# Kernel optimization log

Measured on AMD Instinct MI355X. Metric: run time of the kernel, lower is better.

The kernel has to match this reference:

```python
import jax, jax.numpy as jnp
import numpy as np

LATENT = 10
MAXLEN = 80
DT = 0.1
STEPS = int(round(1.0 / DT))
HIDDEN = 32
BATCH = 512


def _score_fn(xt_bld, time_b1, W1, b1, W2, b2):
    # score_model: flatten (B, L, D) -> concat time -> Dense(32, relu) -> Dense(D)
    B = xt_bld.shape[0]
    h = jnp.concatenate([xt_bld.reshape(B, -1), time_b1], axis=-1)  # (B, L*D+1)
    h = jax.nn.relu(h @ W1 + b1)
    return h @ W2 + b2  # (B, D)


def setup_inputs() -> dict:
    key = jax.random.key(0)
    k1, k2, k3, k4 = jax.random.split(key, 4)
    fan_in = MAXLEN * LATENT + 1  # 801
    z_mean = jax.random.normal(k1, (BATCH, MAXLEN, LATENT), jnp.float32)
    z_log_var = 0.1 * jax.random.normal(k2, (BATCH, MAXLEN, LATENT), jnp.float32)
    W1 = jax.random.normal(k3, (fan_in, HIDDEN), jnp.float32) / np.sqrt(fan_in)
    b1 = jnp.zeros((HIDDEN,), jnp.float32)
    W2 = jax.random.normal(k4, (HIDDEN, LATENT), jnp.float32) / np.sqrt(HIDDEN)
    b2 = jnp.zeros((LATENT,), jnp.float32)
    return {"z_mean": z_mean, "z_log_var": z_log_var, "W1": W1, "b1": b1, "W2": W2, "b2": b2}


def _diffusion_loss(z_mean, z_log_var, W1, b1, W2, b2):
    B = z_mean.shape[0]
    sigma = jnp.exp(z_log_var)                    # ez_log_var in train_step
    mu_tr = jnp.transpose(z_mean, (1, 0, 2))      # (L, B, D)
    sigma_tr = jnp.transpose(sigma, (1, 0, 2))    # (L, B, D)
    zero = jnp.zeros((1, B, LATENT), mu_tr.dtype)
    full_mu_ext = jnp.concatenate([zero, mu_tr], axis=0)       # (L+1, B, D)
    full_sigma_ext = jnp.concatenate([zero, sigma_tr], axis=0)  # (L+1, B, D)
    noise_keys = jax.random.split(jax.random.key(1337), MAXLEN * (STEPS + 1)).reshape(MAXLEN, STEPS + 1)

    def diffusion_step(i, mu_i, sigma_i, keys):
        # mask_below_target_step: keep rows < i
        mask = (jnp.arange(MAXLEN) < i).astype(mu_tr.dtype)[:, None, None]
        masked_mu = mu_tr * mask                                   # (L, B, D)
        times = i.astype(jnp.float32) + jnp.arange(STEPS, dtype=jnp.float32) * DT
        sigma_std = jnp.sqrt(sigma_i)                              # (B, D)
        x0 = mu_i + sigma_std * jax.random.normal(keys[0], (B, LATENT))

        def body(xt, xs):
            t, k = xs
            t_idx = jnp.floor(t).astype(jnp.int32)
            next_mu = jax.lax.dynamic_index_in_dim(full_mu_ext, t_idx + 1, 0, keepdims=False)
            next_sigma = jax.lax.dynamic_index_in_dim(full_sigma_ext, t_idx + 1, 0, keepdims=False)
            one_hot = jax.nn.one_hot(t_idx, MAXLEN, dtype=xt.dtype)     # (L,)
            score_in = masked_mu + one_hot[:, None, None] * xt[None]    # (L, B, D)
            score_in = jnp.transpose(score_in, (1, 0, 2))               # (B, L, D)
            time_col = jnp.full((B, 1), t, xt.dtype)
            score = _score_fn(score_in, time_col, W1, b1, W2, b2)       # (B, D)
            logdx = -(xt - next_mu) / jnp.sqrt(next_sigma)
            err = jnp.abs(logdx - score)
            dW = jax.random.normal(k, (B, LATENT)) * jnp.sqrt(DT)
            xt = xt + 0.5 * jnp.square(sigma_std) * score + sigma_std * dW
            return xt, err

        xt_final, errs = jax.lax.scan(body, x0, (times, keys[1:]))
        return xt_final, errs.sum(axis=0)  # tf.reduce_sum(error, axis=0)

    seq, err = jax.vmap(diffusion_step)(jnp.arange(MAXLEN), mu_tr, sigma_tr, noise_keys)
    sequence = jnp.transpose(seq, (1, 0, 2))       # (B, L, D)
    score_error = jnp.transpose(err, (1, 0, 2))    # (B, L, D)
    return sequence, score_error


def reference(z_mean, z_log_var, W1, b1, W2, b2):
    return _diffusion_loss(z_mean, z_log_var, W1, b1, W2, b2)
```

## Files before the change

### kernel.cpp

```cpp
#include <hip/hip_runtime.h>
#include <stdint.h>

#define LATENT 10
#define MAXLEN 80
#define STEPS  10
#define HIDDEN 32
#define BATCH  512
#define NSEG   16
#define SEGL   5
#define CPB    16
#define TPB    128

__device__ __forceinline__ void tf2x32(uint32_t k0, uint32_t k1,
                                       uint32_t x0, uint32_t x1,
                                       uint32_t& o0, uint32_t& o1) {
  uint32_t ks2 = k0 ^ k1 ^ 0x1BD11BDAu;
  uint32_t v0 = x0 + k0;
  uint32_t v1 = x1 + k1;
#define TF_R(rot) { v0 += v1; v1 = (v1 << (rot)) | (v1 >> (32 - (rot))); v1 ^= v0; }
  TF_R(13) TF_R(15) TF_R(26) TF_R(6)
  v0 += k1;  v1 += ks2 + 1u;
  TF_R(17) TF_R(29) TF_R(16) TF_R(24)
  v0 += ks2; v1 += k0 + 2u;
  TF_R(13) TF_R(15) TF_R(26) TF_R(6)
  v0 += k0;  v1 += k1 + 3u;
  TF_R(17) TF_R(29) TF_R(16) TF_R(24)
  v0 += k1;  v1 += ks2 + 4u;
  TF_R(13) TF_R(15) TF_R(26) TF_R(6)
  v0 += ks2; v1 += k0 + 5u;
#undef TF_R
  o0 = v0; o1 = v1;
}

__device__ __forceinline__ float bits_to_normal(uint32_t bits) {
  const float lo = -0.99999994f;
  float f = __uint_as_float((bits >> 9) | 0x3f800000u) - 1.0f;
  float u = fmaf(f, 2.0f, lo);
  u = fmaxf(u, lo);
  float w = -__logf(fmaf(-u, u, 1.0f));
  float p;
  if (w < 5.0f) {
    w -= 2.5f;
    p = 2.81022636e-08f;
    p = fmaf(p, w, 3.43273939e-07f);
    p = fmaf(p, w, -3.5233877e-06f);
    p = fmaf(p, w, -4.39150654e-06f);
    p = fmaf(p, w, 0.00021858087f);
    p = fmaf(p, w, -0.00125372503f);
    p = fmaf(p, w, -0.00417768164f);
    p = fmaf(p, w, 0.246640727f);
    p = fmaf(p, w, 1.50140941f);
  } else {
    w = sqrtf(w) - 3.0f;
    p = -0.000200214257f;
    p = fmaf(p, w, 0.000100950558f);
    p = fmaf(p, w, 0.00134934322f);
    p = fmaf(p, w, -0.00367342844f);
    p = fmaf(p, w, 0.00573950773f);
    p = fmaf(p, w, -0.0076224613f);
    p = fmaf(p, w, 0.00943887047f);
    p = fmaf(p, w, 1.00167406f);
    p = fmaf(p, w, 2.83297682f);
  }
  return 1.4142135623730951f * (p * u);
}

__global__ __launch_bounds__(256) void k_seg(
    const float* __restrict__ zmean, const float* __restrict__ W1,
    float* __restrict__ segtot) {
  int id = blockIdx.x * 256 + threadIdx.x;
  int s = id >> 14;
  int r = id & 16383;
  int b = r >> 5, j = r & 31;
  float pf0 = 0.0f, pf1 = 0.0f;
#pragma unroll
  for (int t = 0; t < SEGL; ++t) {
    int l = s * SEGL + t;
    const float2* mrow = (const float2*)(zmean + (b * MAXLEN + l) * LATENT);
    float2 m0 = mrow[0], m1 = mrow[1], m2 = mrow[2], m3 = mrow[3], m4 = mrow[4];
    const float* wl = W1 + (l * LATENT) * HIDDEN + j;
    pf0 = fmaf(m0.x, wl[0 * HIDDEN], pf0);
    pf1 = fmaf(m0.y, wl[1 * HIDDEN], pf1);
    pf0 = fmaf(m1.x, wl[2 * HIDDEN], pf0);
    pf1 = fmaf(m1.y, wl[3 * HIDDEN], pf1);
    pf0 = fmaf(m2.x, wl[4 * HIDDEN], pf0);
    pf1 = fmaf(m2.y, wl[5 * HIDDEN], pf1);
    pf0 = fmaf(m3.x, wl[6 * HIDDEN], pf0);
    pf1 = fmaf(m3.y, wl[7 * HIDDEN], pf1);
    pf0 = fmaf(m4.x, wl[8 * HIDDEN], pf0);
    pf1 = fmaf(m4.y, wl[9 * HIDDEN], pf1);
  }
  segtot[(s * BATCH + b) * HIDDEN + j] = pf0 + pf1;
}

__global__ __launch_bounds__(TPB) void k_chain(
    const float* __restrict__ zmean, const float* __restrict__ zlv,
    const float* __restrict__ W1, const float* __restrict__ b1v,
    const float* __restrict__ W2, const float* __restrict__ b2v,
    const float* __restrict__ segtot,
    float* __restrict__ outSeq, float* __restrict__ outErr) {
  __shared__ float nrmS[(STEPS + 1) * LATENT * CPB];
  __shared__ uint32_t skk[2 * (STEPS + 1)];

  const int tid = threadIdx.x;
  const int i = blockIdx.x >> 5;
  const int b0 = (blockIdx.x & 31) << 4;

  if (tid < (STEPS + 1)) {
    uint32_t a, c;
    tf2x32(0u, 1337u, 0u, (uint32_t)(i * (STEPS + 1) + tid), a, c);
    skk[2 * tid] = a; skk[2 * tid + 1] = c;
  }
  __syncthreads();

  const float SQRT_DT = 0.31622776601683794f;
#define GEN_DRAW(IDX)                                                        \
  {                                                                          \
    int c_ = (IDX) & (CPB - 1), n_ = (IDX) >> 4;                             \
    int k_ = (n_ * 205) >> 11;                                               \
    int d_ = n_ - k_ * 10;                                                   \
    uint32_t o0_, o1_;                                                       \
    tf2x32(skk[2 * k_], skk[2 * k_ + 1], 0u,                                 \
           (uint32_t)((b0 + c_) * LATENT + d_), o0_, o1_);                   \
    float v_ = bits_to_normal(o0_ ^ o1_);                                    \
    nrmS[n_ * CPB + c_] = (n_ < LATENT) ? v_ : v_ * SQRT_DT;                 \
  }
#pragma unroll
  for (int rr = 0; rr < 13; ++rr) GEN_DRAW(rr * TPB + tid);
  if (tid < (STEPS + 1) * LATENT * CPB - 13 * TPB) GEN_DRAW(13 * TPB + tid);
#undef GEN_DRAW
  __syncthreads();

  const int r = tid & 7;
  const int jb = r * 4;
  const int cloc = tid >> 3;
  const int b = b0 + cloc;

  const float* rowT = W1 + (MAXLEN * LATENT) * HIDDEN;
  float pf[4], wT[4];
  const float fi = (float)i;
#pragma unroll
  for (int k = 0; k < 4; ++k) {
    wT[k] = rowT[jb + k];
    pf[k] = fmaf(fi, wT[k], b1v[jb + k]);
  }
  const int fs = i / SEGL;
  for (int s2 = 0; s2 < fs; ++s2) {
    float4 t0 = *(const float4*)(segtot + ((size_t)s2 * BATCH + b) * HIDDEN + jb);
    pf[0] += t0.x; pf[1] += t0.y; pf[2] += t0.z; pf[3] += t0.w;
  }
  for (int l = fs * SEGL; l < i; ++l) {
    const float2* mrow = (const float2*)(zmean + (b * MAXLEN + l) * LATENT);
    const float* wl = W1 + (l * LATENT) * HIDDEN + jb;
#pragma unroll
    for (int p = 0; p < 5; ++p) {
      float2 m = mrow[p];
      float4 wa = *(const float4*)(wl + (2 * p) * HIDDEN);
      float4 wb = *(const float4*)(wl + (2 * p + 1) * HIDDEN);
      pf[0] = fmaf(m.x, wa.x, pf[0]); pf[1] = fmaf(m.x, wa.y, pf[1]);
      pf[2] = fmaf(m.x, wa.z, pf[2]); pf[3] = fmaf(m.x, wa.w, pf[3]);
      pf[0] = fmaf(m.y, wb.x, pf[0]); pf[1] = fmaf(m.y, wb.y, pf[1]);
      pf[2] = fmaf(m.y, wb.z, pf[2]); pf[3] = fmaf(m.y, wb.w, pf[3]);
    }
  }

  const int base = (b * MAXLEN + i) * LATENT;
  float mu[LATENT], shalf[LATENT], u[LATENT], errs[LATENT], b2[LATENT];
  float w1s[LATENT][4];
  {
    const float2* zm = (const float2*)(zmean + base);
    const float2* zl = (const float2*)(zlv + base);
    const float* W1i = W1 + (i * LATENT) * HIDDEN + jb;
#pragma unroll
    for (int p = 0; p < 5; ++p) {
      float2 m = zm[p], v = zl[p];
      float s0 = sqrtf(expf(v.x));
      float s1 = sqrtf(expf(v.y));
      mu[2 * p] = m.x; mu[2 * p + 1] = m.y;
      shalf[2 * p] = 0.5f * s0; shalf[2 * p + 1] = 0.5f * s1;
      float4 wa = *(const float4*)(W1i + (2 * p) * HIDDEN);
      float4 wb = *(const float4*)(W1i + (2 * p + 1) * HIDDEN);
      pf[0] = fmaf(m.x, wa.x, pf[0]); pf[1] = fmaf(m.x, wa.y, pf[1]);
      pf[2] = fmaf(m.x, wa.z, pf[2]); pf[3] = fmaf(m.x, wa.w, pf[3]);
      pf[0] = fmaf(m.y, wb.x, pf[0]); pf[1] = fmaf(m.y, wb.y, pf[1]);
      pf[2] = fmaf(m.y, wb.z, pf[2]); pf[3] = fmaf(m.y, wb.w, pf[3]);
      w1s[2 * p][0] = s0 * wa.x; w1s[2 * p][1] = s0 * wa.y;
      w1s[2 * p][2] = s0 * wa.z; w1s[2 * p][3] = s0 * wa.w;
      w1s[2 * p + 1][0] = s1 * wb.x; w1s[2 * p + 1][1] = s1 * wb.y;
      w1s[2 * p + 1][2] = s1 * wb.z; w1s[2 * p + 1][3] = s1 * wb.w;
    }
  }
#pragma unroll
  for (int d = 0; d < LATENT; ++d) {
    b2[d] = b2v[d];
    errs[d] = 0.0f;
    u[d] = nrmS[d * CPB + cloc];
  }

  const float* W2q = W2 + jb * LATENT;

  for (int s = 0; s < STEPS; ++s) {
    float nd[LATENT];
#pragma unroll
    for (int d = 0; d < LATENT; ++d)
      nd[d] = nrmS[((s + 1) * LATENT + d) * CPB + cloc];

    const float ts = (float)s * 0.1f;
    float h[4];
#pragma unroll
    for (int k = 0; k < 4; ++k) h[k] = fmaf(ts, wT[k], pf[k]);
#pragma unroll
    for (int d = 0; d < LATENT; ++d) {
      const float ud = u[d];
      h[0] = fmaf(ud, w1s[d][0], h[0]); h[1] = fmaf(ud, w1s[d][1], h[1]);
      h[2] = fmaf(ud, w1s[d][2], h[2]); h[3] = fmaf(ud, w1s[d][3], h[3]);
    }
    float sc[LATENT];
#pragma unroll
    for (int d = 0; d < LATENT; ++d) sc[d] = 0.0f;
#pragma unroll
    for (int k = 0; k < 4; ++k) {
      const float hj = fmaxf(h[k], 0.0f);
      const float2* w2r = (const float2*)(W2q + k * LATENT);
#pragma unroll
      for (int p = 0; p < 5; ++p) {
        float2 w = w2r[p];
        sc[2 * p] = fmaf(hj, w.x, sc[2 * p]);
        sc[2 * p + 1] = fmaf(hj, w.y, sc[2 * p + 1]);
      }
    }
#pragma unroll
    for (int m = 1; m < 8; m <<= 1) {
#pragma unroll
      for (int d = 0; d < LATENT; ++d) sc[d] += __shfl_xor(sc[d], m);
    }
#pragma unroll
    for (int d = 0; d < LATENT; ++d) {
      float st = sc[d] + b2[d];
      errs[d] += fabsf(u[d] + st);
      u[d] = u[d] + fmaf(shalf[d], st, nd[d]);
    }
  }

#pragma unroll
  for (int d = 0; d < LATENT; ++d) {
    if ((d & 7) == r) {
      float sd = shalf[d] + shalf[d];
      outSeq[base + d] = fmaf(sd, u[d], mu[d]);
      outErr[base + d] = errs[d];
    }
  }
}

__global__ __launch_bounds__(64) void k_mono(
    const float* __restrict__ zmean, const float* __restrict__ zlv,
    const float* __restrict__ W1, const float* __restrict__ b1v,
    const float* __restrict__ W2, const float* __restrict__ b2v,
    float* __restrict__ outSeq, float* __restrict__ outErr) {
  int i = blockIdx.x >> 3;
  int b = ((blockIdx.x & 7) << 6) + threadIdx.x;
  float pref[HIDDEN];
#pragma unroll
  for (int j = 0; j < HIDDEN; ++j) pref[j] = 0.0f;
  for (int l = 0; l < i; ++l) {
    const float* mrow = zmean + (b * MAXLEN + l) * LATENT;
    const float* wrow = W1 + (l * LATENT) * HIDDEN;
#pragma unroll
    for (int d = 0; d < LATENT; ++d) {
      float m = mrow[d];
#pragma unroll
      for (int j = 0; j < HIDDEN; ++j) pref[j] = fmaf(m, wrow[d * HIDDEN + j], pref[j]);
    }
  }
  const int base = (b * MAXLEN + i) * LATENT;
  float mu[LATENT], sstd[LATENT], xt[LATENT], errs[LATENT];
#pragma unroll
  for (int d = 0; d < LATENT; ++d) {
    mu[d] = zmean[base + d];
    sstd[d] = sqrtf(expf(zlv[base + d]));
  }
  float n0[LATENT];
  {
    uint32_t a, c;
    tf2x32(0u, 1337u, 0u, (uint32_t)(i * (STEPS + 1)), a, c);
#pragma unroll
    for (int d = 0; d < LATENT; ++d) {
      uint32_t o0, o1;
      tf2x32(a, c, 0u, (uint32_t)(b * LATENT + d), o0, o1);
      n0[d] = bits_to_normal(o0 ^ o1);
    }
  }
#pragma unroll
  for (int d = 0; d < LATENT; ++d) { xt[d] = mu[d] + sstd[d] * n0[d]; errs[d] = 0.0f; }
  const float* rowT  = W1 + (MAXLEN * LATENT) * HIDDEN;
  const float* rowsI = W1 + (i * LATENT) * HIDDEN;
  const float SQRT_DT = 0.31622776601683794f;
  for (int s = 0; s < STEPS; ++s) {
    float t = (float)i + (float)s * 0.1f;
    float h[HIDDEN];
#pragma unroll
    for (int j = 0; j < HIDDEN; ++j) h[j] = pref[j];
#pragma unroll
    for (int d = 0; d < LATENT; ++d) {
      float xd = xt[d];
      const float* row = rowsI + d * HIDDEN;
#pragma unroll
      for (int j = 0; j < HIDDEN; ++j) h[j] = fmaf(xd, row[j], h[j]);
    }
    float sc[LATENT];
#pragma unroll
    for (int d = 0; d < LATENT; ++d) sc[d] = b2v[d];
#pragma unroll
    for (int j = 0; j < HIDDEN; ++j) {
      float hj = fmaf(t, rowT[j], h[j]) + b1v[j];
      hj = fmaxf(hj, 0.0f);
      const float* w2r = W2 + j * LATENT;
#pragma unroll
      for (int d = 0; d < LATENT; ++d) sc[d] = fmaf(hj, w2r[d], sc[d]);
    }
    float nd[LATENT];
    {
      uint32_t a, c;
      tf2x32(0u, 1337u, 0u, (uint32_t)(i * (STEPS + 1) + s + 1), a, c);
#pragma unroll
      for (int d = 0; d < LATENT; ++d) {
        uint32_t o0, o1;
        tf2x32(a, c, 0u, (uint32_t)(b * LATENT + d), o0, o1);
        nd[d] = bits_to_normal(o0 ^ o1);
      }
    }
#pragma unroll
    for (int d = 0; d < LATENT; ++d) {
      float logdx = -(xt[d] - mu[d]) / sstd[d];
      errs[d] += fabsf(logdx - sc[d]);
      float dW = nd[d] * SQRT_DT;
      xt[d] = xt[d] + (0.5f * (sstd[d] * sstd[d])) * sc[d] + sstd[d] * dW;
    }
  }
#pragma unroll
  for (int d = 0; d < LATENT; ++d) {
    outSeq[base + d] = xt[d];
    outErr[base + d] = errs[d];
  }
}

extern "C" void kernel_launch(void* const* d_in, const int* in_sizes, int n_in,
                              void* d_out, int out_size, void* d_ws, size_t ws_size,
                              hipStream_t stream) {
  (void)in_sizes; (void)n_in; (void)out_size;
  const float* zmean = (const float*)d_in[0];
  const float* zlv   = (const float*)d_in[1];
  const float* W1    = (const float*)d_in[2];
  const float* b1v   = (const float*)d_in[3];
  const float* W2    = (const float*)d_in[4];
  const float* b2v   = (const float*)d_in[5];
  float* outSeq = (float*)d_out;
  float* outErr = outSeq + (size_t)BATCH * MAXLEN * LATENT;

  const size_t segBytes = (size_t)NSEG * BATCH * HIDDEN * sizeof(float);

  if (ws_size >= segBytes) {
    float* segtot = (float*)d_ws;
    hipLaunchKernelGGL(k_seg, dim3(NSEG * BATCH * HIDDEN / 256), dim3(256), 0, stream,
                       zmean, W1, segtot);
    hipLaunchKernelGGL(k_chain, dim3(MAXLEN * (BATCH / CPB)), dim3(TPB), 0, stream,
                       zmean, zlv, W1, b1v, W2, b2v, segtot, outSeq, outErr);
  } else {
    hipLaunchKernelGGL(k_mono, dim3(MAXLEN * 8), dim3(64), 0, stream,
                       zmean, zlv, W1, b1v, W2, b2v, outSeq, outErr);
  }
}
```

Baseline: 104.8 us.

## Replace shuffle butterfly reduction with LDS transpose-reduce and distribute latent ownership

Each group of 8 lanes used to all-reduce 10 score partials with a 3-level xor-shuffle butterfly (30 shuffles per step) and every lane redundantly updated all 10 latent dims. Now each lane writes its partials to shared memory and reads back 8 partials for only the one or two dims it owns, sums them, updates u, and publishes u to shared memory for the next step's hidden-layer accumulation. The per-column sigma is also precomputed once into shared memory rather than recomputed per thread. This trades shuffle traffic and redundant math for LDS round-trips. It relies on the 8 lanes sharing a column being in the same wavefront, since there is no barrier between the LDS writes and reads.

Measured after the change: 100.8 us. 3.8% less time.

```diff
diff --git a/kernel.cpp b/kernel.cpp
--- a/kernel.cpp
+++ b/kernel.cpp
@@ -10,6 +10,9 @@
 #define SEGL   5
 #define CPB    16
 #define TPB    128
+
+#define SCP_STRIDE 84
+#define US_STRIDE  12
 
 __device__ __forceinline__ void tf2x32(uint32_t k0, uint32_t k1,
                                        uint32_t x0, uint32_t x1,
@@ -101,6 +104,9 @@
     float* __restrict__ outSeq, float* __restrict__ outErr) {
   __shared__ float nrmS[(STEPS + 1) * LATENT * CPB];
   __shared__ uint32_t skk[2 * (STEPS + 1)];
+  __shared__ float shS[CPB * LATENT];
+  __shared__ float scP[CPB * SCP_STRIDE];
+  __shared__ float uS[CPB * US_STRIDE];
 
   const int tid = threadIdx.x;
   const int i = blockIdx.x >> 5;
@@ -110,6 +116,10 @@
     uint32_t a, c;
     tf2x32(0u, 1337u, 0u, (uint32_t)(i * (STEPS + 1) + tid), a, c);
     skk[2 * tid] = a; skk[2 * tid + 1] = c;
+  }
+  for (int t = tid; t < CPB * LATENT; t += TPB) {
+    int c_ = t / LATENT, d_ = t - c_ * LATENT;
+    shS[t] = 0.5f * sqrtf(expf(zlv[((b0 + c_) * MAXLEN + i) * LATENT + d_]));
   }
   __syncthreads();
 
@@ -165,19 +175,17 @@
   }
 
   const int base = (b * MAXLEN + i) * LATENT;
-  float mu[LATENT], shalf[LATENT], u[LATENT], errs[LATENT], b2[LATENT];
   float w1s[LATENT][4];
   {
     const float2* zm = (const float2*)(zmean + base);
-    const float2* zl = (const float2*)(zlv + base);
+    const float2* shp = (const float2*)(shS + cloc * LATENT);
     const float* W1i = W1 + (i * LATENT) * HIDDEN + jb;
 #pragma unroll
     for (int p = 0; p < 5; ++p) {
-      float2 m = zm[p], v = zl[p];
-      float s0 = sqrtf(expf(v.x));
-      float s1 = sqrtf(expf(v.y));
-      mu[2 * p] = m.x; mu[2 * p + 1] = m.y;
-      shalf[2 * p] = 0.5f * s0; shalf[2 * p + 1] = 0.5f * s1;
+      float2 m = zm[p];
+      float2 sh = shp[p];
+      float s0 = sh.x + sh.x;
+      float s1 = sh.y + sh.y;
       float4 wa = *(const float4*)(W1i + (2 * p) * HIDDEN);
       float4 wb = *(const float4*)(W1i + (2 * p + 1) * HIDDEN);
       pf[0] = fmaf(m.x, wa.x, pf[0]); pf[1] = fmaf(m.x, wa.y, pf[1]);
@@ -190,37 +198,56 @@
       w1s[2 * p + 1][2] = s1 * wb.z; w1s[2 * p + 1][3] = s1 * wb.w;
     }
   }
-#pragma unroll
-  for (int d = 0; d < LATENT; ++d) {
-    b2[d] = b2v[d];
-    errs[d] = 0.0f;
-    u[d] = nrmS[d * CPB + cloc];
+
+  float sh0 = shS[cloc * LATENT + r];
+  float b2o0 = b2v[r];
+  float u0o = nrmS[r * CPB + cloc];
+  float e0 = 0.0f;
+  float sh1 = 0.0f, b2o1 = 0.0f, u1o = 0.0f, e1 = 0.0f;
+  if (r < 2) {
+    sh1 = shS[cloc * LATENT + 8 + r];
+    b2o1 = b2v[8 + r];
+    u1o = nrmS[(8 + r) * CPB + cloc];
+  }
+  {
+    float* uw = uS + cloc * US_STRIDE;
+    uw[r] = u0o;
+    if (r < 2) uw[8 + r] = u1o;
   }
 
   const float* W2q = W2 + jb * LATENT;
+  float* scw = scP + cloc * SCP_STRIDE + r;
+  const float* scrd0 = scP + cloc * SCP_STRIDE + r * 8;
+  const float* scrd1 = scP + cloc * SCP_STRIDE + (8 + r) * 8;
+  const float2* urd = (const float2*)(uS + cloc * US_STRIDE);
+  const float* ndp = nrmS + LATENT * CPB + cloc;
 
   for (int s = 0; s < STEPS; ++s) {
-    float nd[LATENT];
-#pragma unroll
-    for (int d = 0; d < LATENT; ++d)
-      nd[d] = nrmS[((s + 1) * LATENT + d) * CPB + cloc];
+    float2 ua = urd[0], ub = urd[1], uc = urd[2], ud = urd[3], ue = urd[4];
 
     const float ts = (float)s * 0.1f;
     float h[4];
 #pragma unroll
     for (int k = 0; k < 4; ++k) h[k] = fmaf(ts, wT[k], pf[k]);
-#pragma unroll
-    for (int d = 0; d < LATENT; ++d) {
-      const float ud = u[d];
-      h[0] = fmaf(ud, w1s[d][0], h[0]); h[1] = fmaf(ud, w1s[d][1], h[1]);
-      h[2] = fmaf(ud, w1s[d][2], h[2]); h[3] = fmaf(ud, w1s[d][3], h[3]);
-    }
+#define ACC(d, val) { h[0] = fmaf((val), w1s[d][0], h[0]); h[1] = fmaf((val), w1s[d][1], h[1]); \
+                      h[2] = fmaf((val), w1s[d][2], h[2]); h[3] = fmaf((val), w1s[d][3], h[3]); }
+    ACC(0, ua.x) ACC(1, ua.y) ACC(2, ub.x) ACC(3, ub.y) ACC(4, uc.x)
+    ACC(5, uc.y) ACC(6, ud.x) ACC(7, ud.y) ACC(8, ue.x) ACC(9, ue.y)
+#undef ACC
+
     float sc[LATENT];
-#pragma unroll
-    for (int d = 0; d < LATENT; ++d) sc[d] = 0.0f;
-#pragma unroll
-    for (int k = 0; k < 4; ++k) {
-      const float hj = fmaxf(h[k], 0.0f);
+    {
+      float hj = fmaxf(h[0], 0.0f);
+      const float2* w2r = (const float2*)(W2q);
+#pragma unroll
+      for (int p = 0; p < 5; ++p) {
+        float2 w = w2r[p];
+        sc[2 * p] = hj * w.x; sc[2 * p + 1] = hj * w.y;
+      }
+    }
+#pragma unroll
+    for (int k = 1; k < 4; ++k) {
+      float hj = fmaxf(h[k], 0.0f);
       const float2* w2r = (const float2*)(W2q + k * LATENT);
 #pragma unroll
       for (int p = 0; p < 5; ++p) {
@@ -229,25 +256,46 @@
         sc[2 * p + 1] = fmaf(hj, w.y, sc[2 * p + 1]);
       }
     }
-#pragma unroll
-    for (int m = 1; m < 8; m <<= 1) {
-#pragma unroll
-      for (int d = 0; d < LATENT; ++d) sc[d] += __shfl_xor(sc[d], m);
-    }
-#pragma unroll
-    for (int d = 0; d < LATENT; ++d) {
-      float st = sc[d] + b2[d];
-      errs[d] += fabsf(u[d] + st);
-      u[d] = u[d] + fmaf(shalf[d], st, nd[d]);
-    }
-  }
-
-#pragma unroll
-  for (int d = 0; d < LATENT; ++d) {
-    if ((d & 7) == r) {
-      float sd = shalf[d] + shalf[d];
-      outSeq[base + d] = fmaf(sd, u[d], mu[d]);
-      outErr[base + d] = errs[d];
+
+#pragma unroll
+    for (int d = 0; d < LATENT; ++d) scw[d * 8] = sc[d];
+
+    {
+      float4 lo = *(const float4*)(scrd0);
+      float4 hi = *(const float4*)(scrd0 + 4);
+      float ssum = ((lo.x + lo.y) + (lo.z + lo.w)) +
+                   ((hi.x + hi.y) + (hi.z + hi.w));
+      float st = ssum + b2o0;
+      float ndv = ndp[s * (LATENT * CPB) + r * CPB];
+      e0 += fabsf(u0o + st);
+      u0o = u0o + fmaf(sh0, st, ndv);
+    }
+    if (r < 2) {
+      float4 lo = *(const float4*)(scrd1);
+      float4 hi = *(const float4*)(scrd1 + 4);
+      float ssum = ((lo.x + lo.y) + (lo.z + lo.w)) +
+                   ((hi.x + hi.y) + (hi.z + hi.w));
+      float st = ssum + b2o1;
+      float ndv = ndp[s * (LATENT * CPB) + (8 + r) * CPB];
+      e1 += fabsf(u1o + st);
+      u1o = u1o + fmaf(sh1, st, ndv);
+    }
+
+    {
+      float* uw = uS + cloc * US_STRIDE;
+      uw[r] = u0o;
+      if (r < 2) uw[8 + r] = u1o;
+    }
+  }
+
+  {
+    float sd0 = sh0 + sh0;
+    outSeq[base + r] = fmaf(sd0, u0o, zmean[base + r]);
+    outErr[base + r] = e0;
+    if (r < 2) {
+      float sd1 = sh1 + sh1;
+      outSeq[base + 8 + r] = fmaf(sd1, u1o, zmean[base + 8 + r]);
+      outErr[base + 8 + r] = e1;
     }
   }
 }
```
